# Performance work log

Hardware: AMD Instinct MI355X
Metric: run time of the kernel (lower is better)

Reference implementation:

```python
import jax, jax.numpy as jnp
import numpy as np

D = 32        # number of causal nodes
DF = 256      # d * factor (factor=8)
BATCH = 32768


def setup_inputs() -> dict:
    key = jax.random.key(0)
    ks = jax.random.split(key, 16)
    f32 = jnp.float32

    def w(k, shape, fan_in):
        return (jax.random.normal(k, shape, f32) / np.sqrt(fan_in)).astype(f32)

    return {
        "xor": jax.random.normal(ks[0], (BATCH, D), f32),
        "m": jax.random.normal(ks[1], (BATCH, D), f32),   # unused by the module
        "eps": jax.random.normal(ks[2], (BATCH, D), f32),  # reparameterization noise
        # encoder: enc1 (d->df), enc2 (df->df, 1 extra layer), enc3 (df->2d)
        "We1": w(ks[3], (D, DF), D),   "be1": jnp.zeros((DF,), f32),
        "We2": w(ks[4], (DF, DF), DF), "be2": jnp.zeros((DF,), f32),
        "We3": w(ks[5], (DF, 2 * D), DF), "be3": jnp.zeros((2 * D,), f32),
        # per-node decoder stacks. dec1[i] is Linear(i+1 -> DF); we store it as a
        # full [D, DF] weight per node and mask the inputs (columns > i are masked
        # to zero before the matmul), which is mathematically identical to the
        # ragged gather + small Linear in the original.
        "W1": w(ks[6], (D, D, DF), D),  "b1": jnp.zeros((D, DF), f32),
        "W2": w(ks[7], (D, DF, DF), DF), "b2": jnp.zeros((D, DF), f32),
        "W3": w(ks[8], (D, DF), DF),     "b3": jnp.zeros((D,), f32),
    }


def reference(xor, m, eps, We1, be1, We2, be2, We3, be3, W1, b1, W2, b2, W3, b3):
    d = W1.shape[0]
    # encoder: relu(enc1) -> [Linear->ReLU] -> enc3 -> view(-1, 2, d)
    h = jax.nn.relu(xor @ We1 + be1)
    h = jax.nn.relu(h @ We2 + be2)
    z = (h @ We3 + be3).reshape(-1, 2, d)
    mu = z[:, 0, :]
    log_var = z[:, 1, :]
    y0 = mu + jnp.exp(log_var / 2) * eps  # rsample

    node_idx = jnp.arange(d)

    # sequential decode: node i reads columns B[:, i] = {0..i} of the CURRENT
    # y_recon (earlier nodes already overwritten), then overwrites column i.
    def body(y, i):
        mask = (node_idx <= i).astype(y.dtype)          # parents 0..i-1 plus self
        t = jax.nn.relu((y * mask) @ W1[i] + b1[i])     # [B, DF]
        t = jax.nn.relu(t @ W2[i] + b2[i])              # [B, DF]
        out = t @ W3[i] + b3[i]                         # [B]
        y = y.at[:, i].set(out)
        return y, None

    y, _ = jax.lax.scan(body, y0, jnp.arange(d))
    # no_noise=True: x[:, i] = y_recon[:, i], so x == final y_recon
    return (y, mu, log_var, y)
```

## Files before the change

kernel.cpp:

```cpp
#include <hip/hip_runtime.h>

#define DD 32
#define DFF 256
#define BATCH_N 32768
#define ROWS 64
#define THREADS 256
#define BD (BATCH_N * DD)
#define YPITCH 40
#define YFP 33

typedef __bf16 bf16x8 __attribute__((ext_vector_type(8)));
typedef __bf16 bf16x4 __attribute__((ext_vector_type(4)));
typedef float f32x4 __attribute__((ext_vector_type(4)));

__device__ __forceinline__ unsigned short f2bf(float f) {
  unsigned int u = __builtin_bit_cast(unsigned int, f);
  u += 0x7FFFu + ((u >> 16) & 1u);
  return (unsigned short)(u >> 16);
}

__global__ void repack_kernel(const float* __restrict__ src,
                              unsigned short* __restrict__ dst,
                              int K, int N, long sstride, long dstride) {
  long mat = blockIdx.y;
  int p = blockIdx.x * 256 + threadIdx.x;
  if (p >= K * N) return;
  int NT = N >> 4;
  int j = p & 7;
  int l = (p >> 3) & 63;
  int rest = p >> 9;
  int nt = rest % NT;
  int ks = rest / NT;
  int k = ks * 32 + ((l >> 4) << 3) + j;
  int n = nt * 16 + (l & 15);
  dst[mat * dstride + p] = f2bf(src[mat * sstride + (long)k * N + n]);
}

__device__ __forceinline__ int swzA(int row, int col) {
  return ((row * DFF + col) * 2) ^ ((row & 7) << 4);
}
__device__ __forceinline__ bf16x8 ldA(const unsigned short* buf, int row, int k0) {
  return __builtin_bit_cast(bf16x8, *(const uint4*)((const char*)buf + swzA(row, k0)));
}
__device__ __forceinline__ bf16x8 ldY(const unsigned short* ybf, int row, int k0) {
  return __builtin_bit_cast(bf16x8, *(const uint4*)(ybf + row * YPITCH + k0));
}
__device__ __forceinline__ uint4 ldWraw(const unsigned short* __restrict__ wp,
                                        int ks, int NT, int ntAbs, int lane) {
  return *(const uint4*)(wp + ((((ks * NT + ntAbs) << 6) + lane) << 3));
}
__device__ __forceinline__ bf16x8 asw(uint4 v) { return __builtin_bit_cast(bf16x8, v); }

#define MFMA16(a, b, c) __builtin_amdgcn_mfma_f32_16x16x32_bf16((a), (b), (c), 0, 0, 0)

__device__ __forceinline__ void biasInit(f32x4 acc[4][4], const float* __restrict__ b,
                                         int ng, int lg) {
#pragma unroll
  for (int nt = 0; nt < 4; ++nt) {
    f32x4 bv = *(const f32x4*)(b + (ng * 4 + nt) * 16 + lg * 4);
#pragma unroll
    for (int rt = 0; rt < 4; ++rt) acc[nt][rt] = bv;
  }
}

__device__ __forceinline__ void storeAct(unsigned short* act, f32x4 acc[4][4],
                                         int ng, int lr, int lg) {
#pragma unroll
  for (int nt = 0; nt < 4; ++nt) {
    int n = (ng * 4 + nt) * 16 + lg * 4;
#pragma unroll
    for (int rt = 0; rt < 4; ++rt) {
      int r = rt * 16 + lr;
      bf16x4 w;
#pragma unroll
      for (int rr = 0; rr < 4; ++rr) w[rr] = (__bf16)fmaxf(acc[nt][rt][rr], 0.f);
      *(bf16x4*)((char*)act + swzA(r, n)) = w;
    }
  }
}

__global__ __launch_bounds__(THREADS, 2)
void vae_kernel(const float* __restrict__ xin, const float* __restrict__ eps,
                const float* __restrict__ be1, const float* __restrict__ be2,
                const float* __restrict__ be3, const float* __restrict__ b1,
                const float* __restrict__ b2, const float* __restrict__ W3,
                const float* __restrict__ b3,
                const unsigned short* __restrict__ We1p,
                const unsigned short* __restrict__ We2p,
                const unsigned short* __restrict__ We3p,
                const unsigned short* __restrict__ W1p,
                const unsigned short* __restrict__ W2p,
                float* __restrict__ out) {
  __shared__ __align__(16) unsigned short act[ROWS * DFF];
  __shared__ unsigned short ybf[ROWS * YPITCH];
  __shared__ float yf[ROWS * YFP];
  __shared__ float red[4 * ROWS];

  {
    unsigned units = ((blockIdx.x >> 8) & 1) * 2 + ((blockIdx.x >> 3) & 1);
    for (unsigned s = 0; s < units; ++s) __builtin_amdgcn_s_sleep(63);
  }

  const int tid = threadIdx.x;
  const int lane = tid & 63;
  const int ng = tid >> 6;
  const int lr = lane & 15;
  const int lg = lane >> 4;
  const long r0 = (long)blockIdx.x * ROWS;

  for (int e = tid; e < ROWS * DD; e += THREADS) {
    int rr = e >> 5, d = e & 31;
    ybf[rr * YPITCH + d] = f2bf(xin[(r0 + rr) * DD + d]);
  }
  __syncthreads();

  f32x4 acc[4][4];

  biasInit(acc, be1, ng, lg);
  {
    bf16x8 yb[4];
#pragma unroll
    for (int rt = 0; rt < 4; ++rt) yb[rt] = ldY(ybf, rt * 16 + lr, lg * 8);
#pragma unroll
    for (int nt = 0; nt < 4; ++nt) {
      bf16x8 w = asw(ldWraw(We1p, 0, 16, ng * 4 + nt, lane));
#pragma unroll
      for (int rt = 0; rt < 4; ++rt) acc[nt][rt] = MFMA16(w, yb[rt], acc[nt][rt]);
    }
  }
  storeAct(act, acc, ng, lr, lg);
  __syncthreads();

  biasInit(acc, be2, ng, lg);
#pragma unroll
  for (int ks = 0; ks < 8; ++ks) {
    bf16x8 ab[4];
#pragma unroll
    for (int rt = 0; rt < 4; ++rt) ab[rt] = ldA(act, rt * 16 + lr, ks * 32 + lg * 8);
#pragma unroll
    for (int nt = 0; nt < 4; ++nt) {
      bf16x8 w = asw(ldWraw(We2p, ks, 16, ng * 4 + nt, lane));
#pragma unroll
      for (int rt = 0; rt < 4; ++rt) acc[nt][rt] = MFMA16(w, ab[rt], acc[nt][rt]);
    }
  }
  __syncthreads();
  storeAct(act, acc, ng, lr, lg);
  __syncthreads();

  {
    f32x4 az[4];
    f32x4 bz = *(const f32x4*)(be3 + ng * 16 + lg * 4);
#pragma unroll
    for (int rt = 0; rt < 4; ++rt) az[rt] = bz;
#pragma unroll
    for (int ks = 0; ks < 8; ++ks) {
      bf16x8 w = asw(ldWraw(We3p, ks, 4, ng, lane));
#pragma unroll
      for (int rt = 0; rt < 4; ++rt) {
        bf16x8 a = ldA(act, rt * 16 + lr, ks * 32 + lg * 8);
        az[rt] = MFMA16(w, a, az[rt]);
      }
    }
    __syncthreads();
    float* zt = (float*)act;
#pragma unroll
    for (int rt = 0; rt < 4; ++rt) {
      int r = rt * 16 + lr;
#pragma unroll
      for (int rr = 0; rr < 4; ++rr)
        zt[(ng * 16 + lg * 4 + rr) * 66 + r] = az[rt][rr];
    }
  }
  __syncthreads();

  {
    const float* zt = (const float*)act;
    for (int e = tid; e < ROWS * DD; e += THREADS) {
      int rr = e >> 5, d = e & 31;
      float mu = zt[d * 66 + rr];
      float lv = zt[(32 + d) * 66 + rr];
      long gi = (r0 + rr) * DD + d;
      float y0 = mu + __expf(0.5f * lv) * eps[gi];
      yf[rr * YFP + d] = y0;
      ybf[rr * YPITCH + d] = (d == 0) ? f2bf(y0) : (unsigned short)0;
      out[BD + gi] = mu;
      out[2L * BD + gi] = lv;
    }
  }

  uint4 w1f[4], w2f[4][4];
#pragma unroll
  for (int nt = 0; nt < 4; ++nt) w1f[nt] = ldWraw(W1p, 0, 16, ng * 4 + nt, lane);
#pragma unroll
  for (int ks = 0; ks < 4; ++ks)
#pragma unroll
    for (int nt = 0; nt < 4; ++nt) w2f[ks][nt] = ldWraw(W2p, ks, 16, ng * 4 + nt, lane);
  __syncthreads();

#pragma unroll 1
  for (int i = 0; i < DD; ++i) {
    const unsigned short* W2cur = W2p + i * (DFF * DFF);
    const int inx = (i + 1 < DD) ? i + 1 : i;
    const unsigned short* W1nx = W1p + inx * (DD * DFF);
    const unsigned short* W2nx = W2p + inx * (DFF * DFF);

    biasInit(acc, b1 + i * DFF, ng, lg);
    {
      bf16x8 yb[4];
#pragma unroll
      for (int rt = 0; rt < 4; ++rt) yb[rt] = ldY(ybf, rt * 16 + lr, lg * 8);
#pragma unroll
      for (int nt = 0; nt < 4; ++nt) {
        bf16x8 w = asw(w1f[nt]);
#pragma unroll
        for (int rt = 0; rt < 4; ++rt) acc[nt][rt] = MFMA16(w, yb[rt], acc[nt][rt]);
      }
    }
    storeAct(act, acc, ng, lr, lg);
    __syncthreads();

    biasInit(acc, b2 + i * DFF, ng, lg);
#pragma unroll
    for (int ks = 0; ks < 4; ++ks) {
      bf16x8 ab[4];
#pragma unroll
      for (int rt = 0; rt < 4; ++rt) ab[rt] = ldA(act, rt * 16 + lr, ks * 32 + lg * 8);
#pragma unroll
      for (int nt = 0; nt < 4; ++nt) {
        bf16x8 w = asw(w2f[ks][nt]);
#pragma unroll
        for (int rt = 0; rt < 4; ++rt) acc[nt][rt] = MFMA16(w, ab[rt], acc[nt][rt]);
        w2f[ks][nt] = ldWraw(W2cur, ks + 4, 16, ng * 4 + nt, lane);
      }
    }
#pragma unroll
    for (int ks = 4; ks < 8; ++ks) {
      bf16x8 ab[4];
#pragma unroll
      for (int rt = 0; rt < 4; ++rt) ab[rt] = ldA(act, rt * 16 + lr, ks * 32 + lg * 8);
#pragma unroll
      for (int nt = 0; nt < 4; ++nt) {
        bf16x8 w = asw(w2f[ks - 4][nt]);
#pragma unroll
        for (int rt = 0; rt < 4; ++rt) acc[nt][rt] = MFMA16(w, ab[rt], acc[nt][rt]);
        w2f[ks - 4][nt] = ldWraw(W2nx, ks - 4, 16, ng * 4 + nt, lane);
      }
    }
#pragma unroll
    for (int nt = 0; nt < 4; ++nt) w1f[nt] = ldWraw(W1nx, 0, 16, ng * 4 + nt, lane);

    const float* w3r = W3 + i * DFF;
    float part[4] = {0.f, 0.f, 0.f, 0.f};
#pragma unroll
    for (int nt = 0; nt < 4; ++nt) {
      f32x4 w3v = *(const f32x4*)(w3r + (ng * 4 + nt) * 16 + lg * 4);
#pragma unroll
      for (int rt = 0; rt < 4; ++rt)
#pragma unroll
        for (int rr = 0; rr < 4; ++rr)
          part[rt] = fmaf(fmaxf(acc[nt][rt][rr], 0.f), w3v[rr], part[rt]);
    }
#pragma unroll
    for (int rt = 0; rt < 4; ++rt) {
      part[rt] += __shfl_xor(part[rt], 16);
      part[rt] += __shfl_xor(part[rt], 32);
    }
    if (lg == 0) {
#pragma unroll
      for (int rt = 0; rt < 4; ++rt) red[ng * ROWS + rt * 16 + lr] = part[rt];
    }
    __syncthreads();

    if (tid < ROWS) {
      float v = b3[i] + red[tid] + red[ROWS + tid] + red[2 * ROWS + tid] + red[3 * ROWS + tid];
      yf[tid * YFP + i] = v;
      ybf[tid * YPITCH + i] = f2bf(v);
      if (i + 1 < DD)
        ybf[tid * YPITCH + i + 1] = f2bf(yf[tid * YFP + i + 1]);
    }
    __syncthreads();
  }

  for (int e = tid; e < ROWS * DD; e += THREADS) {
    int rr = e >> 5, d = e & 31;
    long gi = (r0 + rr) * DD + d;
    float v = yf[rr * YFP + d];
    out[gi] = v;
    out[3L * BD + gi] = v;
  }
}

extern "C" void kernel_launch(void* const* d_in, const int* in_sizes, int n_in,
                              void* d_out, int out_size, void* d_ws, size_t ws_size,
                              hipStream_t stream) {
  const float* xin = (const float*)d_in[0];
  const float* eps = (const float*)d_in[2];
  const float* We1 = (const float*)d_in[3];
  const float* be1 = (const float*)d_in[4];
  const float* We2 = (const float*)d_in[5];
  const float* be2 = (const float*)d_in[6];
  const float* We3 = (const float*)d_in[7];
  const float* be3 = (const float*)d_in[8];
  const float* W1  = (const float*)d_in[9];
  const float* b1  = (const float*)d_in[10];
  const float* W2  = (const float*)d_in[11];
  const float* b2  = (const float*)d_in[12];
  const float* W3  = (const float*)d_in[13];
  const float* b3  = (const float*)d_in[14];
  float* out = (float*)d_out;

  unsigned short* We1p = (unsigned short*)d_ws;
  unsigned short* We2p = We1p + 32 * 256;
  unsigned short* We3p = We2p + 256 * 256;
  unsigned short* W1p  = We3p + 256 * 64;
  unsigned short* W2p  = W1p + 32 * 32 * 256;

  repack_kernel<<<dim3(32, 1), 256, 0, stream>>>(We1, We1p, 32, 256, 0, 0);
  repack_kernel<<<dim3(256, 1), 256, 0, stream>>>(We2, We2p, 256, 256, 0, 0);
  repack_kernel<<<dim3(64, 1), 256, 0, stream>>>(We3, We3p, 256, 64, 0, 0);
  repack_kernel<<<dim3(32, 32), 256, 0, stream>>>(W1, W1p, 32, 256, 32 * 256, 32 * 256);
  repack_kernel<<<dim3(256, 32), 256, 0, stream>>>(W2, W2p, 256, 256, 256 * 256, 256 * 256);

  vae_kernel<<<dim3(BATCH_N / ROWS), THREADS, 0, stream>>>(
      xin, eps, be1, be2, be3, b1, b2, W3, b3, We1p, We2p, We3p, W1p, W2p, out);
}
```

Measured before the change: 203.9 us.

## Switch decoder loop matmuls from 16x16x32 to 32x32x16 bf16 MFMA

The per-node decoder layers now use the 32x32x16 MFMA instruction instead of 16x16x32, with each wave owning 2x2 32x32 output tiles. W1 and W2 weights are repacked into a new fragment layout to match, and the register prefetch pipeline, bias init, activation store and W3 reduction are rewritten for the new accumulator layout. The goal is higher MFMA throughput per instruction and fewer operand loads from LDS for the same work. The W3 reduction needs only one shuffle step instead of two. The risk is more register pressure from 16-wide accumulators, and a different LDS access pattern for the swizzled activation buffer.

```diff
diff --git a/kernel.cpp b/kernel.cpp
--- a/kernel.cpp
+++ b/kernel.cpp
@@ -12,6 +12,7 @@
 typedef __bf16 bf16x8 __attribute__((ext_vector_type(8)));
 typedef __bf16 bf16x4 __attribute__((ext_vector_type(4)));
 typedef float f32x4 __attribute__((ext_vector_type(4)));
+typedef float f32x16 __attribute__((ext_vector_type(16)));
 
 __device__ __forceinline__ unsigned short f2bf(float f) {
   unsigned int u = __builtin_bit_cast(unsigned int, f);
@@ -21,18 +22,27 @@
 
 __global__ void repack_kernel(const float* __restrict__ src,
                               unsigned short* __restrict__ dst,
-                              int K, int N, long sstride, long dstride) {
+                              int K, int N, long sstride, long dstride, int mode) {
   long mat = blockIdx.y;
   int p = blockIdx.x * 256 + threadIdx.x;
   if (p >= K * N) return;
-  int NT = N >> 4;
   int j = p & 7;
   int l = (p >> 3) & 63;
   int rest = p >> 9;
-  int nt = rest % NT;
-  int ks = rest / NT;
-  int k = ks * 32 + ((l >> 4) << 3) + j;
-  int n = nt * 16 + (l & 15);
+  int k, n;
+  if (mode == 0) {
+    int NT = N >> 4;
+    int nt = rest % NT;
+    int ks = rest / NT;
+    k = ks * 32 + ((l >> 4) << 3) + j;
+    n = nt * 16 + (l & 15);
+  } else {
+    int NT = N >> 5;
+    int nt = rest % NT;
+    int ks = rest / NT;
+    k = ks * 16 + ((l >> 5) << 3) + j;
+    n = nt * 32 + (l & 31);
+  }
   dst[mat * dstride + p] = f2bf(src[mat * sstride + (long)k * N + n]);
 }
 
@@ -52,6 +62,7 @@
 __device__ __forceinline__ bf16x8 asw(uint4 v) { return __builtin_bit_cast(bf16x8, v); }
 
 #define MFMA16(a, b, c) __builtin_amdgcn_mfma_f32_16x16x32_bf16((a), (b), (c), 0, 0, 0)
+#define MFMA32(a, b, c) __builtin_amdgcn_mfma_f32_32x32x16_bf16((a), (b), (c), 0, 0, 0)
 
 __device__ __forceinline__ void biasInit(f32x4 acc[4][4], const float* __restrict__ b,
                                          int ng, int lg) {
@@ -62,7 +73,6 @@
     for (int rt = 0; rt < 4; ++rt) acc[nt][rt] = bv;
   }
 }
-
 __device__ __forceinline__ void storeAct(unsigned short* act, f32x4 acc[4][4],
                                          int ng, int lr, int lg) {
 #pragma unroll
@@ -75,6 +85,40 @@
 #pragma unroll
       for (int rr = 0; rr < 4; ++rr) w[rr] = (__bf16)fmaxf(acc[nt][rt][rr], 0.f);
       *(bf16x4*)((char*)act + swzA(r, n)) = w;
+    }
+  }
+}
+
+__device__ __forceinline__ void biasInit32(f32x16 acc2[2][2], const float* __restrict__ b,
+                                           int ng, int hi) {
+#pragma unroll
+  for (int nt = 0; nt < 2; ++nt) {
+    f32x16 v;
+#pragma unroll
+    for (int g = 0; g < 4; ++g) {
+      f32x4 bv = *(const f32x4*)(b + ng * 64 + nt * 32 + hi * 4 + g * 8);
+#pragma unroll
+      for (int c = 0; c < 4; ++c) v[g * 4 + c] = bv[c];
+    }
+    acc2[nt][0] = v;
+    acc2[nt][1] = v;
+  }
+}
+__device__ __forceinline__ void storeAct32(unsigned short* act, f32x16 acc2[2][2],
+                                           int ng, int hi, int lane) {
+#pragma unroll
+  for (int nt = 0; nt < 2; ++nt) {
+#pragma unroll
+    for (int rt = 0; rt < 2; ++rt) {
+      int r = rt * 32 + (lane & 31);
+#pragma unroll
+      for (int g = 0; g < 4; ++g) {
+        int f = ng * 64 + nt * 32 + hi * 4 + g * 8;
+        bf16x4 w;
+#pragma unroll
+        for (int c = 0; c < 4; ++c) w[c] = (__bf16)fmaxf(acc2[nt][rt][g * 4 + c], 0.f);
+        *(bf16x4*)((char*)act + swzA(r, f)) = w;
+      }
     }
   }
 }
@@ -106,6 +150,7 @@
   const int ng = tid >> 6;
   const int lr = lane & 15;
   const int lg = lane >> 4;
+  const int hi = lane >> 5;
   const long r0 = (long)blockIdx.x * ROWS;
 
   for (int e = tid; e < ROWS * DD; e += THREADS) {
@@ -189,13 +234,15 @@
     }
   }
 
-  uint4 w1f[4], w2f[4][4];
-#pragma unroll
-  for (int nt = 0; nt < 4; ++nt) w1f[nt] = ldWraw(W1p, 0, 16, ng * 4 + nt, lane);
-#pragma unroll
-  for (int ks = 0; ks < 4; ++ks)
-#pragma unroll
-    for (int nt = 0; nt < 4; ++nt) w2f[ks][nt] = ldWraw(W2p, ks, 16, ng * 4 + nt, lane);
+  uint4 w1f[2][2], w2f[8][2];
+#pragma unroll
+  for (int ks = 0; ks < 2; ++ks)
+#pragma unroll
+    for (int nt = 0; nt < 2; ++nt) w1f[ks][nt] = ldWraw(W1p, ks, 8, ng * 2 + nt, lane);
+#pragma unroll
+  for (int ks = 0; ks < 8; ++ks)
+#pragma unroll
+    for (int nt = 0; nt < 2; ++nt) w2f[ks][nt] = ldWraw(W2p, ks, 8, ng * 2 + nt, lane);
   __syncthreads();
 
 #pragma unroll 1
@@ -205,70 +252,83 @@
     const unsigned short* W1nx = W1p + inx * (DD * DFF);
     const unsigned short* W2nx = W2p + inx * (DFF * DFF);
 
-    biasInit(acc, b1 + i * DFF, ng, lg);
+    f32x16 acc2[2][2];
+
+    biasInit32(acc2, b1 + i * DFF, ng, hi);
     {
-      bf16x8 yb[4];
-#pragma unroll
-      for (int rt = 0; rt < 4; ++rt) yb[rt] = ldY(ybf, rt * 16 + lr, lg * 8);
-#pragma unroll
-      for (int nt = 0; nt < 4; ++nt) {
-        bf16x8 w = asw(w1f[nt]);
-#pragma unroll
-        for (int rt = 0; rt < 4; ++rt) acc[nt][rt] = MFMA16(w, yb[rt], acc[nt][rt]);
-      }
-    }
-    storeAct(act, acc, ng, lr, lg);
+      bf16x8 yb[2][2];
+#pragma unroll
+      for (int ks = 0; ks < 2; ++ks)
+#pragma unroll
+        for (int rt = 0; rt < 2; ++rt)
+          yb[ks][rt] = ldY(ybf, rt * 32 + (lane & 31), ks * 16 + hi * 8);
+#pragma unroll
+      for (int ks = 0; ks < 2; ++ks)
+#pragma unroll
+        for (int nt = 0; nt < 2; ++nt) {
+          bf16x8 w = asw(w1f[ks][nt]);
+#pragma unroll
+          for (int rt = 0; rt < 2; ++rt)
+            acc2[nt][rt] = MFMA32(w, yb[ks][rt], acc2[nt][rt]);
+        }
+    }
+    storeAct32(act, acc2, ng, hi, lane);
     __syncthreads();
 
-    biasInit(acc, b2 + i * DFF, ng, lg);
-#pragma unroll
-    for (int ks = 0; ks < 4; ++ks) {
-      bf16x8 ab[4];
-#pragma unroll
-      for (int rt = 0; rt < 4; ++rt) ab[rt] = ldA(act, rt * 16 + lr, ks * 32 + lg * 8);
-#pragma unroll
-      for (int nt = 0; nt < 4; ++nt) {
+    biasInit32(acc2, b2 + i * DFF, ng, hi);
+#pragma unroll
+    for (int ks = 0; ks < 8; ++ks) {
+      bf16x8 ab[2];
+#pragma unroll
+      for (int rt = 0; rt < 2; ++rt)
+        ab[rt] = ldA(act, rt * 32 + (lane & 31), ks * 16 + hi * 8);
+#pragma unroll
+      for (int nt = 0; nt < 2; ++nt) {
         bf16x8 w = asw(w2f[ks][nt]);
 #pragma unroll
-        for (int rt = 0; rt < 4; ++rt) acc[nt][rt] = MFMA16(w, ab[rt], acc[nt][rt]);
-        w2f[ks][nt] = ldWraw(W2cur, ks + 4, 16, ng * 4 + nt, lane);
-      }
-    }
-#pragma unroll
-    for (int ks = 4; ks < 8; ++ks) {
-      bf16x8 ab[4];
-#pragma unroll
-      for (int rt = 0; rt < 4; ++rt) ab[rt] = ldA(act, rt * 16 + lr, ks * 32 + lg * 8);
-#pragma unroll
-      for (int nt = 0; nt < 4; ++nt) {
-        bf16x8 w = asw(w2f[ks - 4][nt]);
-#pragma unroll
-        for (int rt = 0; rt < 4; ++rt) acc[nt][rt] = MFMA16(w, ab[rt], acc[nt][rt]);
-        w2f[ks - 4][nt] = ldWraw(W2nx, ks - 4, 16, ng * 4 + nt, lane);
-      }
-    }
-#pragma unroll
-    for (int nt = 0; nt < 4; ++nt) w1f[nt] = ldWraw(W1nx, 0, 16, ng * 4 + nt, lane);
+        for (int rt = 0; rt < 2; ++rt) acc2[nt][rt] = MFMA32(w, ab[rt], acc2[nt][rt]);
+        w2f[ks][nt] = ldWraw(W2cur, ks + 8, 8, ng * 2 + nt, lane);
+      }
+    }
+#pragma unroll
+    for (int ks = 8; ks < 16; ++ks) {
+      bf16x8 ab[2];
+#pragma unroll
+      for (int rt = 0; rt < 2; ++rt)
+        ab[rt] = ldA(act, rt * 32 + (lane & 31), ks * 16 + hi * 8);
+#pragma unroll
+      for (int nt = 0; nt < 2; ++nt) {
+        bf16x8 w = asw(w2f[ks - 8][nt]);
+#pragma unroll
+        for (int rt = 0; rt < 2; ++rt) acc2[nt][rt] = MFMA32(w, ab[rt], acc2[nt][rt]);
+        w2f[ks - 8][nt] = ldWraw(W2nx, ks - 8, 8, ng * 2 + nt, lane);
+      }
+    }
+#pragma unroll
+    for (int ks = 0; ks < 2; ++ks)
+#pragma unroll
+      for (int nt = 0; nt < 2; ++nt) w1f[ks][nt] = ldWraw(W1nx, ks, 8, ng * 2 + nt, lane);
 
     const float* w3r = W3 + i * DFF;
-    float part[4] = {0.f, 0.f, 0.f, 0.f};
-#pragma unroll
-    for (int nt = 0; nt < 4; ++nt) {
-      f32x4 w3v = *(const f32x4*)(w3r + (ng * 4 + nt) * 16 + lg * 4);
-#pragma unroll
-      for (int rt = 0; rt < 4; ++rt)
-#pragma unroll
-        for (int rr = 0; rr < 4; ++rr)
-          part[rt] = fmaf(fmaxf(acc[nt][rt][rr], 0.f), w3v[rr], part[rt]);
-    }
-#pragma unroll
-    for (int rt = 0; rt < 4; ++rt) {
-      part[rt] += __shfl_xor(part[rt], 16);
-      part[rt] += __shfl_xor(part[rt], 32);
-    }
-    if (lg == 0) {
-#pragma unroll
-      for (int rt = 0; rt < 4; ++rt) red[ng * ROWS + rt * 16 + lr] = part[rt];
+    float part[2] = {0.f, 0.f};
+#pragma unroll
+    for (int nt = 0; nt < 2; ++nt) {
+#pragma unroll
+      for (int g = 0; g < 4; ++g) {
+        f32x4 w3v = *(const f32x4*)(w3r + ng * 64 + nt * 32 + hi * 4 + g * 8);
+#pragma unroll
+        for (int c = 0; c < 4; ++c) {
+#pragma unroll
+          for (int rt = 0; rt < 2; ++rt)
+            part[rt] = fmaf(fmaxf(acc2[nt][rt][g * 4 + c], 0.f), w3v[c], part[rt]);
+        }
+      }
+    }
+#pragma unroll
+    for (int rt = 0; rt < 2; ++rt) part[rt] += __shfl_xor(part[rt], 32);
+    if (lane < 32) {
+#pragma unroll
+      for (int rt = 0; rt < 2; ++rt) red[ng * ROWS + rt * 32 + lane] = part[rt];
     }
     __syncthreads();
 
@@ -316,11 +376,11 @@
   unsigned short* W1p  = We3p + 256 * 64;
   unsigned short* W2p  = W1p + 32 * 32 * 256;
 
-  repack_kernel<<<dim3(32, 1), 256, 0, stream>>>(We1, We1p, 32, 256, 0, 0);
-  repack_kernel<<<dim3(256, 1), 256, 0, stream>>>(We2, We2p, 256, 256, 0, 0);
-  repack_kernel<<<dim3(64, 1), 256, 0, stream>>>(We3, We3p, 256, 64, 0, 0);
-  repack_kernel<<<dim3(32, 32), 256, 0, stream>>>(W1, W1p, 32, 256, 32 * 256, 32 * 256);
-  repack_kernel<<<dim3(256, 32), 256, 0, stream>>>(W2, W2p, 256, 256, 256 * 256, 256 * 256);
+  repack_kernel<<<dim3(32, 1), 256, 0, stream>>>(We1, We1p, 32, 256, 0, 0, 0);
+  repack_kernel<<<dim3(256, 1), 256, 0, stream>>>(We2, We2p, 256, 256, 0, 0, 0);
+  repack_kernel<<<dim3(64, 1), 256, 0, stream>>>(We3, We3p, 256, 64, 0, 0, 0);
+  repack_kernel<<<dim3(32, 32), 256, 0, stream>>>(W1, W1p, 32, 256, 32 * 256, 32 * 256, 1);
+  repack_kernel<<<dim3(256, 32), 256, 0, stream>>>(W2, W2p, 256, 256, 256 * 256, 256 * 256, 1);
 
   vae_kernel<<<dim3(BATCH_N / ROWS), THREADS, 0, stream>>>(
       xin, eps, be1, be2, be3, b1, b2, W3, b3, We1p, We2p, We3p, W1p, W2p, out);
```

Result: slower. 219.9 us (+7.9%).
